# Performance work log

Hardware: AMD Instinct MI355X
Metric: run time of the kernel (lower is better)

## Reference

```python
import jax, jax.numpy as jnp
import numpy as np

EPS = 1e-6      # flax LayerNorm default epsilon
DECAY = 0.1
LOG_ALPHA = 3.5


def _ln(x):
    # flax LayerNorm(reduction_axes=-2, use_bias=False, use_scale=False):
    # normalize over the token axis (-2), no affine params
    mu = x.mean(-2, keepdims=True)
    var = x.var(-2, keepdims=True)
    return (x - mu) * jax.lax.rsqrt(var + EPS)


def setup_inputs() -> dict:
    key = jax.random.key(0)
    ks = jax.random.split(key, 10)
    N, D, H, V = 4096, 64, 256, 8192
    xcat = jax.random.normal(ks[0], (N, D), jnp.float32)
    xsep = jnp.sort(jax.random.randint(ks[1], (N,), 0, 16)).astype(jnp.int32)
    xdiv = jax.random.randint(ks[2], (N,), 0, 2).astype(jnp.int32)
    esti = jax.random.normal(ks[3], (2, N, V), jnp.float32)
    output = jax.random.normal(ks[4], (D, V), jnp.float32) * 0.05
    # module params (init: normal(0.1) for delta/a/b, lecun_normal for Dense)
    delta = jax.random.normal(ks[5], (D, 1), jnp.float32) * 0.1
    a_p = jax.random.normal(ks[6], (D, 1), jnp.float32) * 0.1
    b_p = jax.random.normal(ks[7], (D, D), jnp.float32) * 0.1
    ffn_w1 = jax.random.normal(ks[8], (D, H), jnp.float32) * (1.0 / np.sqrt(D))
    ffn_b1 = jnp.zeros((H,), jnp.float32)
    ffn_w2 = jax.random.normal(ks[9], (H, D), jnp.float32) * (1.0 / np.sqrt(H))
    ffn_b2 = jnp.zeros((D,), jnp.float32)
    return dict(xcat=xcat, esti=esti, output=output, delta=delta, a_p=a_p,
                b_p=b_p, ffn_w1=ffn_w1, ffn_b1=ffn_b1, ffn_w2=ffn_w2,
                ffn_b2=ffn_b2, xsep=xsep, xdiv=xdiv, seed=0)


def reference(xcat, esti, output, delta, a_p, b_p, ffn_w1, ffn_b1, ffn_w2,
              ffn_b2, xsep, xdiv, seed):
    key = jax.random.key(seed)
    key, subkey = jax.random.split(key)
    # randomly drop dividers with prob DECAY
    xdiv = xdiv * (jax.random.uniform(subkey, xdiv.shape) > DECAY)
    t = jax.nn.log_sigmoid(xcat @ delta)  # [N,1] per-token "time"

    def op(x, y):
        xv, xt, xs, xd = x
        yv, yt, ys, yd = y
        dt = (yt - xt)[..., None]                         # [n,1,1]
        A = jnp.exp(dt * a_p) * b_p                       # [n,D,D] decay matrix
        m = ((xs == ys) & (xd == yd)).astype(xv.dtype)    # [n,1] segment mask
        return (yv + m * jnp.einsum('nd,nde->ne', xv, A), yt, ys, yd)

    div_id = xdiv.cumsum(0)[:, None]                      # [N,1]
    xnew, _, _, _ = jax.lax.associative_scan(
        op, (xcat, t, xsep[:, None], div_id), reverse=True, axis=0)

    # ffn = LN(axis=-2) -> Dense(H) -> relu -> Dense(D), residual with xcat
    h = _ln(xnew)
    h = jax.nn.relu(h @ ffn_w1 + ffn_b1) @ ffn_w2 + ffn_b2
    xnew = h + xcat

    xest = jax.nn.log_softmax(_ln(xnew) @ output, axis=-1)  # [N,V]
    gt = (esti[0].max(-1, keepdims=True) > LOG_ALPHA).astype(xest.dtype)  # [N,1]
    esti_new = jnp.stack([gt * esti[0] + (1 - gt) * xest,
                          gt * esti[1] + (1 - gt) * esti[0]], axis=0)
    return (xnew, esti_new)
```

## Files before the change

kernel.cpp:

```cpp
#include <hip/hip_runtime.h>
#include <stdint.h>

#define NN 4096
#define DD 64
#define HH 256
#define VV 8192
#define NVv ((size_t)NN*(size_t)VV)

__device__ __forceinline__ uint32_t rotl32(uint32_t v, int r){ return (v<<r)|(v>>(32-r)); }
#define TF_ROUND(r) do { x0 += x1; x1 = rotl32(x1, r); x1 ^= x0; } while(0)
__device__ __forceinline__ void threefry2x32(uint32_t k0, uint32_t k1,
                                             uint32_t c0, uint32_t c1,
                                             uint32_t& o0, uint32_t& o1){
  uint32_t ks2 = k0 ^ k1 ^ 0x1BD11BDAu;
  uint32_t x0 = c0 + k0, x1 = c1 + k1;
  TF_ROUND(13); TF_ROUND(15); TF_ROUND(26); TF_ROUND(6);
  x0 += k1;  x1 += ks2 + 1u;
  TF_ROUND(17); TF_ROUND(29); TF_ROUND(16); TF_ROUND(24);
  x0 += ks2; x1 += k0 + 2u;
  TF_ROUND(13); TF_ROUND(15); TF_ROUND(26); TF_ROUND(6);
  x0 += k0;  x1 += k1 + 3u;
  TF_ROUND(17); TF_ROUND(29); TF_ROUND(16); TF_ROUND(24);
  x0 += k1;  x1 += ks2 + 4u;
  TF_ROUND(13); TF_ROUND(15); TF_ROUND(26); TF_ROUND(6);
  x0 += ks2; x1 += k0 + 5u;
  o0 = x0; o1 = x1;
}

__global__ __launch_bounds__(64) void k_t(const float* __restrict__ xcat,
                                          const float* __restrict__ delta,
                                          float* __restrict__ t){
  __shared__ float xr[64*65];
  __shared__ float dl[64];
  int b = blockIdx.x, tid = threadIdx.x;
  dl[tid] = delta[tid];
  const float4* src = (const float4*)(xcat + (size_t)b*4096);
  for (int i = tid; i < 1024; i += 64) {
    float4 v = src[i];
    int r = i >> 4, c = (i & 15)*4;
    float* p = &xr[r*65 + c];
    p[0]=v.x; p[1]=v.y; p[2]=v.z; p[3]=v.w;
  }
  __syncthreads();
  float acc = 0.f;
  #pragma unroll 16
  for (int d = 0; d < 64; ++d) acc = fmaf(xr[tid*65 + d], dl[d], acc);
  t[b*64 + tid] = fminf(acc, 0.f) - log1pf(expf(-fabsf(acc)));
}

__global__ __launch_bounds__(256) void k_rng(const int* __restrict__ xdiv,
                                             const int* __restrict__ seedp,
                                             int* __restrict__ dv){
  __shared__ int md[NN];
  __shared__ int ps[256];
  int tid = threadIdx.x;
  uint32_t seed = (uint32_t)seedp[0];
  uint32_t sk0, sk1;
  threefry2x32(0u, seed, 0u, 1u, sk0, sk1);
  for (int i = tid; i < NN; i += 256) {
    uint32_t o0, o1; threefry2x32(sk0, sk1, 0u, (uint32_t)i, o0, o1);
    uint32_t bits = o0 ^ o1;
    float u = __uint_as_float((bits>>9)|0x3f800000u) - 1.0f;
    md[i] = (u > 0.1f) ? xdiv[i] : 0;
  }
  __syncthreads();
  int base = tid*16, s = 0;
  #pragma unroll
  for (int k=0;k<16;k++){ s += md[base+k]; md[base+k] = s; }
  ps[tid] = s;
  __syncthreads();
  if (tid < 64) {
    int a0 = ps[4*tid], a1 = ps[4*tid+1], a2 = ps[4*tid+2], a3 = ps[4*tid+3];
    int s4 = a0+a1+a2+a3;
    int v = s4;
    #pragma unroll
    for (int o = 1; o < 64; o <<= 1) { int u = __shfl_up(v, o, 64); if (tid >= o) v += u; }
    int e = v - s4;
    ps[4*tid] = e; ps[4*tid+1] = e+a0; ps[4*tid+2] = e+a0+a1; ps[4*tid+3] = e+a0+a1+a2;
  }
  __syncthreads();
  int off = ps[tid];
  #pragma unroll
  for (int k=0;k<16;k++) dv[base+k] = md[base+k] + off;
}

__device__ __forceinline__ void wave_combine(const float* __restrict__ Xv,
                                             const float* __restrict__ Yv,
                                             float* __restrict__ Ov,
                                             int bidx, int cidx, int lane,
                                             const float* __restrict__ t,
                                             const int* __restrict__ sep,
                                             const int* __restrict__ dv,
                                             const float* __restrict__ al,
                                             const float* __restrict__ bl){
  int eb = (NN-1) - bidx, ec = (NN-1) - cidx;
  float acc = Yv[lane];
  if (sep[eb] == sep[ec] && dv[eb] == dv[ec]) {
    float dt = t[ec] - t[eb];
    float w = Xv[lane] * expf(dt * al[lane]);
    #pragma unroll 16
    for (int d = 0; d < 64; ++d)
      acc = fmaf(__shfl(w, d, 64), bl[d*64 + lane], acc);
  }
  Ov[lane] = acc;
}

__global__ __launch_bounds__(1024) void k_up(const float* __restrict__ xcat,
    const float* __restrict__ t, const int* __restrict__ sep, const int* __restrict__ dv,
    const float* __restrict__ ap, const float* __restrict__ bp, float* __restrict__ g7){
  __shared__ float G[255*64];
  __shared__ float bl[64*64];
  __shared__ float al[64];
  int b = blockIdx.x, tid = threadIdx.x, lane = tid & 63, wv = tid >> 6;
  for (int i = tid; i < 4096; i += 1024) bl[i] = bp[i];
  if (tid < 64) al[tid] = ap[tid];
  for (int k = wv; k < 128; k += 16) G[k*64 + lane] = xcat[(NN-1 - (128*b + k))*DD + lane];
  __syncthreads();
  const int Gof[8] = {0,128,192,224,240,248,252,254};
  for (int L = 1; L <= 7; ++L) {
    int nc = 128 >> L, s = 1 << (L-1);
    for (int c = wv; c < nc; c += 16)
      wave_combine(&G[(Gof[L-1]+2*c)*64], &G[(Gof[L-1]+2*c+1)*64], &G[(Gof[L]+c)*64],
                   128*b + (2*c+1)*s - 1, 128*b + (2*c+2)*s - 1, lane, t, sep, dv, al, bl);
    __syncthreads();
  }
  if (tid < 64) g7[b*64 + tid] = G[254*64 + tid];
}

__global__ __launch_bounds__(1024) void k_mid(const float* __restrict__ t,
    const int* __restrict__ sep, const int* __restrict__ dv,
    const float* __restrict__ ap, const float* __restrict__ bp,
    const float* __restrict__ g7, float* __restrict__ s7){
  __shared__ float G[63*64];
  __shared__ float R[63*64];
  __shared__ float bl[64*64];
  __shared__ float al[64];
  int tid = threadIdx.x, lane = tid & 63, wv = tid >> 6;
  for (int i = tid; i < 4096; i += 1024) bl[i] = bp[i];
  if (tid < 64) al[tid] = ap[tid];
  for (int k = wv; k < 32; k += 16) G[k*64 + lane] = g7[k*64 + lane];
  __syncthreads();
  const int Gof[13] = {0,0,0,0,0,0,0, 0,32,48,56,60,62};
  const int Rof[13] = {0,0,0,0,0,0,0, 31,15,7,3,1,0};
  for (int l = 8; l <= 12; ++l) {
    int nc = 1 << (12 - l), s = 1 << (l - 1);
    for (int c = wv; c < nc; c += 16)
      wave_combine(&G[(Gof[l-1]+2*c)*64], &G[(Gof[l-1]+2*c+1)*64], &G[(Gof[l]+c)*64],
                   (2*c+1)*s - 1, (2*c+2)*s - 1, lane, t, sep, dv, al, bl);
    __syncthreads();
  }
  if (tid < 64) R[Rof[12]*64 + tid] = G[Gof[12]*64 + tid];
  __syncthreads();
  for (int l = 11; l >= 7; --l) {
    int nL = 1 << (12 - l);
    for (int p = wv; p < nL; p += 16) {
      float* Ov = &R[(Rof[l]+p)*64];
      if (p == 0)        Ov[lane] = G[Gof[l]*64 + lane];
      else if (p & 1)    Ov[lane] = R[(Rof[l+1] + ((p-1)>>1))*64 + lane];
      else wave_combine(&R[(Rof[l+1] + (p>>1) - 1)*64], &G[(Gof[l]+p)*64], Ov,
                        p*(1<<l) - 1, (p+1)*(1<<l) - 1, lane, t, sep, dv, al, bl);
    }
    __syncthreads();
  }
  for (int k = wv; k < 32; k += 16) s7[k*64 + lane] = R[(31+k)*64 + lane];
}

__global__ __launch_bounds__(1024) void k_down(const float* __restrict__ xcat,
    const float* __restrict__ t, const int* __restrict__ sep, const int* __restrict__ dv,
    const float* __restrict__ ap, const float* __restrict__ bp,
    const float* __restrict__ s7, float* __restrict__ xs){
  __shared__ float G[254*64];
  __shared__ float R[255*64];
  __shared__ float bl[64*64];
  __shared__ float al[64];
  __shared__ float s7p[64];
  int b = blockIdx.x, tid = threadIdx.x, lane = tid & 63, wv = tid >> 6;
  for (int i = tid; i < 4096; i += 1024) bl[i] = bp[i];
  if (tid < 64) al[tid] = ap[tid];
  if (tid < 64) R[tid] = s7[b*64 + tid];
  if (tid >= 64 && tid < 128) s7p[tid-64] = (b > 0) ? s7[(b-1)*64 + (tid-64)] : 0.f;
  for (int k = wv; k < 128; k += 16) G[k*64 + lane] = xcat[(NN-1 - (128*b + k))*DD + lane];
  __syncthreads();
  const int Gof[7] = {0,128,192,224,240,248,252};
  const int Rof[8] = {127,63,31,15,7,3,1,0};
  for (int L = 1; L <= 6; ++L) {
    int nc = 128 >> L, s = 1 << (L-1);
    for (int c = wv; c < nc; c += 16)
      wave_combine(&G[(Gof[L-1]+2*c)*64], &G[(Gof[L-1]+2*c+1)*64], &G[(Gof[L]+c)*64],
                   128*b + (2*c+1)*s - 1, 128*b + (2*c+2)*s - 1, lane, t, sep, dv, al, bl);
    __syncthreads();
  }
  for (int L = 6; L >= 0; --L) {
    int nL = 1 << (7 - L);
    for (int p = wv; p < nL; p += 16) {
      float* Ov = &R[(Rof[L]+p)*64];
      int j = b*nL + p;
      if (j == 0)        Ov[lane] = G[Gof[L]*64 + lane];
      else if (p & 1)    Ov[lane] = R[(Rof[L+1] + ((p-1)>>1))*64 + lane];
      else {
        const float* Xv = (p == 0) ? s7p : &R[(Rof[L+1] + (p>>1) - 1)*64];
        wave_combine(Xv, &G[(Gof[L]+p)*64], Ov, j*(1<<L) - 1, (j+1)*(1<<L) - 1,
                     lane, t, sep, dv, al, bl);
      }
    }
    __syncthreads();
  }
  for (int p = wv; p < 128; p += 16)
    xs[(NN-1 - (128*b + p))*DD + lane] = R[(127+p)*64 + lane];
}

__global__ __launch_bounds__(256) void k_stats_part(const float* __restrict__ x,
                                                    float* __restrict__ part){
  __shared__ float s1[256], s2[256];
  int tid = threadIdx.x, d = tid & 63, r = tid >> 6, b = blockIdx.x;
  int n0 = b*16;
  float a = 0.f, q = 0.f;
  #pragma unroll
  for (int k = 0; k < 4; ++k) {
    float v = x[(n0 + r + 4*k)*DD + d];
    a += v; q = fmaf(v, v, q);
  }
  s1[tid] = a; s2[tid] = q;
  __syncthreads();
  if (tid < 64) {
    part[(b*2+0)*64 + tid] = s1[tid] + s1[tid+64] + s1[tid+128] + s1[tid+192];
    part[(b*2+1)*64 + tid] = s2[tid] + s2[tid+64] + s2[tid+128] + s2[tid+192];
  }
}

__global__ __launch_bounds__(256) void k_stats_fin(const float* __restrict__ part,
                                                   float* __restrict__ mu,
                                                   float* __restrict__ rs){
  __shared__ float s1[256], s2[256];
  int tid = threadIdx.x, d = tid & 63, p = tid >> 6;
  float a = 0.f, q = 0.f;
  #pragma unroll 8
  for (int i = p; i < 256; i += 4) {
    a += part[(i*2+0)*64 + d];
    q += part[(i*2+1)*64 + d];
  }
  s1[tid] = a; s2[tid] = q;
  __syncthreads();
  if (tid < 64) {
    float S = s1[tid]+s1[tid+64]+s1[tid+128]+s1[tid+192];
    float Q = s2[tid]+s2[tid+64]+s2[tid+128]+s2[tid+192];
    float m = S/(float)NN;
    float var = fmaxf(Q/(float)NN - m*m, 0.f);
    mu[tid] = m; rs[tid] = rsqrtf(var + 1e-6f);
  }
}

__global__ __launch_bounds__(256) void k_ffn(const float* __restrict__ xs,
    const float* __restrict__ xcat, const float* __restrict__ mu, const float* __restrict__ rs,
    const float* __restrict__ w1, const float* __restrict__ b1,
    const float* __restrict__ w2, const float* __restrict__ b2,
    float* __restrict__ xnew){
  __shared__ float xln[16*64];
  __shared__ float Hl[16*HH];
  int b = blockIdx.x, tid = threadIdx.x;
  int n0 = b*16;
  for (int idx = tid; idx < 1024; idx += 256) {
    int i = idx >> 6, d = idx & 63;
    xln[idx] = (xs[(n0+i)*DD + d] - mu[d]) * rs[d];
  }
  float w1c[64];
  #pragma unroll
  for (int d = 0; d < 64; ++d) w1c[d] = w1[d*HH + tid];
  float bb1 = b1[tid];
  __syncthreads();
  #pragma unroll 2
  for (int i = 0; i < 16; ++i) {
    float acc = bb1;
    #pragma unroll
    for (int d = 0; d < 64; ++d) acc = fmaf(xln[i*64 + d], w1c[d], acc);
    Hl[i*HH + tid] = fmaxf(acc, 0.f);
  }
  __syncthreads();
  int e = tid & 63, ig = tid >> 6;
  for (int k = 0; k < 4; ++k) {
    int i = ig + 4*k;
    float acc = b2[e];
    #pragma unroll 8
    for (int h = 0; h < HH; ++h) acc = fmaf(Hl[i*HH + h], w2[h*DD + e], acc);
    int n = n0 + i;
    xnew[n*DD + e] = acc + xcat[n*DD + e];
  }
}

#define FMA4(Z,W) do { Z.x=fmaf(xv,W.x,Z.x); Z.y=fmaf(xv,W.y,Z.y); \
                       Z.z=fmaf(xv,W.z,Z.z); Z.w=fmaf(xv,W.w,Z.w); } while(0)
#define MAX4(M,V) M = fmaxf(M, fmaxf(fmaxf(V.x,V.y), fmaxf(V.z,V.w)))
__global__ __launch_bounds__(256)
__attribute__((amdgpu_waves_per_eu(2, 4)))
void k_est(const float* __restrict__ xnew,
    const float* __restrict__ mu, const float* __restrict__ rs,
    const float* __restrict__ outw, const float* __restrict__ esti,
    float* __restrict__ dout){
  __shared__ float xl[64];
  __shared__ float r4a[4], r4b[4], r4c[4];
  int n = blockIdx.x, tid = threadIdx.x, lane = tid & 63, wv = tid >> 6;
  const float4* e0 = (const float4*)(esti + (size_t)n*VV);
  const float4* e1 = (const float4*)(esti + NVv + (size_t)n*VV);
  float4* o0 = (float4*)(dout + (size_t)NN*DD + (size_t)n*VV);
  float4* o1 = (float4*)(dout + (size_t)NN*DD + NVv + (size_t)n*VV);
  if (tid < 64) xl[tid] = (xnew[n*DD + tid] - mu[tid]) * rs[tid];
  float4 a0 = e0[tid],        a1 = e0[tid + 256],  a2 = e0[tid + 512],  a3 = e0[tid + 768];
  float4 a4 = e0[tid + 1024], a5 = e0[tid + 1280], a6 = e0[tid + 1536], a7 = e0[tid + 1792];
  float mx = -1e30f;
  MAX4(mx,a0); MAX4(mx,a1); MAX4(mx,a2); MAX4(mx,a3);
  MAX4(mx,a4); MAX4(mx,a5); MAX4(mx,a6); MAX4(mx,a7);
  #pragma unroll
  for (int o = 32; o; o >>= 1) mx = fmaxf(mx, __shfl_xor(mx, o, 64));
  if (lane == 0) r4a[wv] = mx;
  __syncthreads();
  float m0 = fmaxf(fmaxf(r4a[0], r4a[1]), fmaxf(r4a[2], r4a[3]));
  if (m0 > 3.5f) {
    o0[tid]        = a0; o0[tid + 256]  = a1; o0[tid + 512]  = a2; o0[tid + 768]  = a3;
    o0[tid + 1024] = a4; o0[tid + 1280] = a5; o0[tid + 1536] = a6; o0[tid + 1792] = a7;
    float4 b0 = e1[tid],        b1 = e1[tid + 256],  b2 = e1[tid + 512],  b3 = e1[tid + 768];
    float4 b4 = e1[tid + 1024], b5 = e1[tid + 1280], b6 = e1[tid + 1536], b7 = e1[tid + 1792];
    o1[tid]        = b0; o1[tid + 256]  = b1; o1[tid + 512]  = b2; o1[tid + 768]  = b3;
    o1[tid + 1024] = b4; o1[tid + 1280] = b5; o1[tid + 1536] = b6; o1[tid + 1792] = b7;
    return;
  }
  o1[tid]        = a0; o1[tid + 256]  = a1; o1[tid + 512]  = a2; o1[tid + 768]  = a3;
  o1[tid + 1024] = a4; o1[tid + 1280] = a5; o1[tid + 1536] = a6; o1[tid + 1792] = a7;
  float4 z00 = make_float4(0,0,0,0), z01 = make_float4(0,0,0,0);
  float4 z02 = make_float4(0,0,0,0), z03 = make_float4(0,0,0,0);
  for (int d = 0; d < 64; ++d) {
    float xv = xl[d];
    const float4* wr = (const float4*)(outw + (size_t)d*VV) + tid;
    float4 w0 = wr[0], w1 = wr[256], w2 = wr[512], w3 = wr[768];
    FMA4(z00,w0); FMA4(z01,w1); FMA4(z02,w2); FMA4(z03,w3);
  }
  float4 z10 = make_float4(0,0,0,0), z11 = make_float4(0,0,0,0);
  float4 z12 = make_float4(0,0,0,0), z13 = make_float4(0,0,0,0);
  for (int d = 0; d < 64; ++d) {
    float xv = xl[d];
    const float4* wr = (const float4*)(outw + (size_t)d*VV) + tid + 1024;
    float4 w0 = wr[0], w1 = wr[256], w2 = wr[512], w3 = wr[768];
    FMA4(z10,w0); FMA4(z11,w1); FMA4(z12,w2); FMA4(z13,w3);
  }
  float zmax = -1e30f;
  MAX4(zmax,z00); MAX4(zmax,z01); MAX4(zmax,z02); MAX4(zmax,z03);
  MAX4(zmax,z10); MAX4(zmax,z11); MAX4(zmax,z12); MAX4(zmax,z13);
  #pragma unroll
  for (int o = 32; o; o >>= 1) zmax = fmaxf(zmax, __shfl_xor(zmax, o, 64));
  if (lane == 0) r4b[wv] = zmax;
  __syncthreads();
  zmax = fmaxf(fmaxf(r4b[0], r4b[1]), fmaxf(r4b[2], r4b[3]));
  float s = 0.f;
  #define SUM4(V) s += expf(V.x - zmax) + expf(V.y - zmax) + expf(V.z - zmax) + expf(V.w - zmax)
  SUM4(z00); SUM4(z01); SUM4(z02); SUM4(z03);
  SUM4(z10); SUM4(z11); SUM4(z12); SUM4(z13);
  #undef SUM4
  #pragma unroll
  for (int o = 32; o; o >>= 1) s += __shfl_xor(s, o, 64);
  if (lane == 0) r4c[wv] = s;
  __syncthreads();
  float lse = zmax + logf(r4c[0] + r4c[1] + r4c[2] + r4c[3]);
  #define STO(Z,OFF) do { float4 v=Z; v.x-=lse; v.y-=lse; v.z-=lse; v.w-=lse; o0[OFF]=v; } while(0)
  STO(z00, tid);        STO(z01, tid + 256);  STO(z02, tid + 512);  STO(z03, tid + 768);
  STO(z10, tid + 1024); STO(z11, tid + 1280); STO(z12, tid + 1536); STO(z13, tid + 1792);
  #undef STO
}

extern "C" void kernel_launch(void* const* d_in, const int* in_sizes, int n_in,
                              void* d_out, int out_size, void* d_ws, size_t ws_size,
                              hipStream_t stream) {
  const float* xcat = (const float*)d_in[0];
  const float* esti = (const float*)d_in[1];
  const float* outw = (const float*)d_in[2];
  const float* delta= (const float*)d_in[3];
  const float* ap   = (const float*)d_in[4];
  const float* bp   = (const float*)d_in[5];
  const float* w1   = (const float*)d_in[6];
  const float* b1   = (const float*)d_in[7];
  const float* w2   = (const float*)d_in[8];
  const float* b2   = (const float*)d_in[9];
  const int* xsep   = (const int*)d_in[10];
  const int* xdiv   = (const int*)d_in[11];
  const int* seedp  = (const int*)d_in[12];
  float* out = (float*)d_out;

  char* ws = (char*)d_ws;
  float* t    = (float*)(ws);
  int*   dv   = (int*)  (ws + 16384);
  float* g7   = (float*)(ws + 32768);
  float* s7   = (float*)(ws + 40960);
  float* xs   = (float*)(ws + 49152);
  float* mu1  = (float*)(ws + 49152 + 1048576);
  float* rs1  = mu1 + 64;
  float* mu2  = rs1 + 64;
  float* rs2  = mu2 + 64;
  float* part = (float*)(ws + 49152 + 1048576 + 4096);

  hipLaunchKernelGGL(k_t,          dim3(64),   dim3(64),   0, stream, xcat, delta, t);
  hipLaunchKernelGGL(k_rng,        dim3(1),    dim3(256),  0, stream, xdiv, seedp, dv);
  hipLaunchKernelGGL(k_up,         dim3(32),   dim3(1024), 0, stream, xcat, t, xsep, dv, ap, bp, g7);
  hipLaunchKernelGGL(k_mid,        dim3(1),    dim3(1024), 0, stream, t, xsep, dv, ap, bp, g7, s7);
  hipLaunchKernelGGL(k_down,       dim3(32),   dim3(1024), 0, stream, xcat, t, xsep, dv, ap, bp, s7, xs);
  hipLaunchKernelGGL(k_stats_part, dim3(256),  dim3(256),  0, stream, xs, part);
  hipLaunchKernelGGL(k_stats_fin,  dim3(1),    dim3(256),  0, stream, part, mu1, rs1);
  hipLaunchKernelGGL(k_ffn,        dim3(256),  dim3(256),  0, stream, xs, xcat, mu1, rs1, w1, b1, w2, b2, out);
  hipLaunchKernelGGL(k_stats_part, dim3(256),  dim3(256),  0, stream, out, part);
  hipLaunchKernelGGL(k_stats_fin,  dim3(1),    dim3(256),  0, stream, part, mu2, rs2);
  hipLaunchKernelGGL(k_est,        dim3(NN),   dim3(256),  0, stream, out, mu2, rs2, outw, esti, out);
}
```

Baseline: 295.5 us.

## Split estimate kernel into flag, streaming select-copy, and skip-flagged GEMV kernels

The fused per-row estimate kernel is split into three kernels. k_flag computes each row's max over esti[0]. k_sel then does a grid-strided float4 select-copy of both esti planes into the output. k_gemv runs the projection and log-softmax only for unflagged rows, exiting early otherwise. The aim is a clean streaming copy kernel and a GEMV freed from the esti loads. The cost is a second full read of esti[0] and two extra launches.

```diff
diff --git a/kernel.cpp b/kernel.cpp
--- a/kernel.cpp
+++ b/kernel.cpp
@@ -287,44 +287,56 @@
   }
 }
 
+#define MAX4(M,V) M = fmaxf(M, fmaxf(fmaxf(V.x,V.y), fmaxf(V.z,V.w)))
 #define FMA4(Z,W) do { Z.x=fmaf(xv,W.x,Z.x); Z.y=fmaf(xv,W.y,Z.y); \
                        Z.z=fmaf(xv,W.z,Z.z); Z.w=fmaf(xv,W.w,Z.w); } while(0)
-#define MAX4(M,V) M = fmaxf(M, fmaxf(fmaxf(V.x,V.y), fmaxf(V.z,V.w)))
-__global__ __launch_bounds__(256)
-__attribute__((amdgpu_waves_per_eu(2, 4)))
-void k_est(const float* __restrict__ xnew,
+
+__global__ __launch_bounds__(256) void k_flag(const float* __restrict__ esti,
+                                              int* __restrict__ flag){
+  int wid = (blockIdx.x << 2) + (threadIdx.x >> 6);
+  int lane = threadIdx.x & 63;
+  const float4* e0 = (const float4*)(esti + (size_t)wid*VV);
+  float mx = -1e30f;
+  #pragma unroll 8
+  for (int j = 0; j < 32; ++j) {
+    float4 v = e0[lane + 64*j];
+    MAX4(mx, v);
+  }
+  #pragma unroll
+  for (int o = 32; o; o >>= 1) mx = fmaxf(mx, __shfl_xor(mx, o, 64));
+  if (lane == 0) flag[wid] = (mx > 3.5f) ? 1 : 0;
+}
+
+__global__ __launch_bounds__(256) void k_sel(const float* __restrict__ esti,
+                                             const int* __restrict__ flag,
+                                             float* __restrict__ dout){
+  const float4* e0 = (const float4*)esti;
+  const float4* e1 = (const float4*)(esti + NVv);
+  float4* o0 = (float4*)(dout + (size_t)NN*DD);
+  float4* o1 = (float4*)(dout + (size_t)NN*DD + NVv);
+  size_t base = (size_t)blockIdx.x*256 + threadIdx.x;
+  #pragma unroll 4
+  for (int k = 0; k < 16; ++k) {
+    size_t g = base + (size_t)k*524288;
+    int n = (int)(g >> 11);
+    float4 x = e0[g];
+    if (flag[n]) { o0[g] = x; o1[g] = e1[g]; }
+    else o1[g] = x;
+  }
+}
+
+__global__ __launch_bounds__(256) void k_gemv(const float* __restrict__ xnew,
     const float* __restrict__ mu, const float* __restrict__ rs,
-    const float* __restrict__ outw, const float* __restrict__ esti,
+    const float* __restrict__ outw, const int* __restrict__ flag,
     float* __restrict__ dout){
+  int n = blockIdx.x;
+  if (flag[n]) return;
   __shared__ float xl[64];
-  __shared__ float r4a[4], r4b[4], r4c[4];
-  int n = blockIdx.x, tid = threadIdx.x, lane = tid & 63, wv = tid >> 6;
-  const float4* e0 = (const float4*)(esti + (size_t)n*VV);
-  const float4* e1 = (const float4*)(esti + NVv + (size_t)n*VV);
+  __shared__ float r4b[4], r4c[4];
+  int tid = threadIdx.x, lane = tid & 63, wv = tid >> 6;
   float4* o0 = (float4*)(dout + (size_t)NN*DD + (size_t)n*VV);
-  float4* o1 = (float4*)(dout + (size_t)NN*DD + NVv + (size_t)n*VV);
   if (tid < 64) xl[tid] = (xnew[n*DD + tid] - mu[tid]) * rs[tid];
-  float4 a0 = e0[tid],        a1 = e0[tid + 256],  a2 = e0[tid + 512],  a3 = e0[tid + 768];
-  float4 a4 = e0[tid + 1024], a5 = e0[tid + 1280], a6 = e0[tid + 1536], a7 = e0[tid + 1792];
-  float mx = -1e30f;
-  MAX4(mx,a0); MAX4(mx,a1); MAX4(mx,a2); MAX4(mx,a3);
-  MAX4(mx,a4); MAX4(mx,a5); MAX4(mx,a6); MAX4(mx,a7);
-  #pragma unroll
-  for (int o = 32; o; o >>= 1) mx = fmaxf(mx, __shfl_xor(mx, o, 64));
-  if (lane == 0) r4a[wv] = mx;
-  __syncthreads();
-  float m0 = fmaxf(fmaxf(r4a[0], r4a[1]), fmaxf(r4a[2], r4a[3]));
-  if (m0 > 3.5f) {
-    o0[tid]        = a0; o0[tid + 256]  = a1; o0[tid + 512]  = a2; o0[tid + 768]  = a3;
-    o0[tid + 1024] = a4; o0[tid + 1280] = a5; o0[tid + 1536] = a6; o0[tid + 1792] = a7;
-    float4 b0 = e1[tid],        b1 = e1[tid + 256],  b2 = e1[tid + 512],  b3 = e1[tid + 768];
-    float4 b4 = e1[tid + 1024], b5 = e1[tid + 1280], b6 = e1[tid + 1536], b7 = e1[tid + 1792];
-    o1[tid]        = b0; o1[tid + 256]  = b1; o1[tid + 512]  = b2; o1[tid + 768]  = b3;
-    o1[tid + 1024] = b4; o1[tid + 1280] = b5; o1[tid + 1536] = b6; o1[tid + 1792] = b7;
-    return;
-  }
-  o1[tid]        = a0; o1[tid + 256]  = a1; o1[tid + 512]  = a2; o1[tid + 768]  = a3;
-  o1[tid + 1024] = a4; o1[tid + 1280] = a5; o1[tid + 1536] = a6; o1[tid + 1792] = a7;
+  __syncthreads();
   float4 z00 = make_float4(0,0,0,0), z01 = make_float4(0,0,0,0);
   float4 z02 = make_float4(0,0,0,0), z03 = make_float4(0,0,0,0);
   for (int d = 0; d < 64; ++d) {
@@ -394,7 +406,10 @@
   float* mu2  = rs1 + 64;
   float* rs2  = mu2 + 64;
   float* part = (float*)(ws + 49152 + 1048576 + 4096);
-
+  int*   flag = (int*)  (ws + 49152 + 1048576 + 4096 + 131072);
+
+  hipLaunchKernelGGL(k_flag,       dim3(1024), dim3(256),  0, stream, esti, flag);
+  hipLaunchKernelGGL(k_sel,        dim3(2048), dim3(256),  0, stream, esti, flag, out);
   hipLaunchKernelGGL(k_t,          dim3(64),   dim3(64),   0, stream, xcat, delta, t);
   hipLaunchKernelGGL(k_rng,        dim3(1),    dim3(256),  0, stream, xdiv, seedp, dv);
   hipLaunchKernelGGL(k_up,         dim3(32),   dim3(1024), 0, stream, xcat, t, xsep, dv, ap, bp, g7);
@@ -405,5 +420,5 @@
   hipLaunchKernelGGL(k_ffn,        dim3(256),  dim3(256),  0, stream, xs, xcat, mu1, rs1, w1, b1, w2, b2, out);
   hipLaunchKernelGGL(k_stats_part, dim3(256),  dim3(256),  0, stream, out, part);
   hipLaunchKernelGGL(k_stats_fin,  dim3(1),    dim3(256),  0, stream, part, mu2, rs2);
-  hipLaunchKernelGGL(k_est,        dim3(NN),   dim3(256),  0, stream, out, mu2, rs2, outw, esti, out);
-}
+  hipLaunchKernelGGL(k_gemv,       dim3(NN),   dim3(256),  0, stream, out, mu2, rs2, outw, flag, out);
+}
```

New measurement: 327.3 us. +10.8%, slower.
